# Optimization experiments

Hardware: AMD Instinct MI355X
Metric: run time of the kernel (lower is better)

The kernel has to match this reference:

```python
import jax, jax.numpy as jnp
import numpy as np

EMBEDDING_DIM = 128
NEG = -1000.0


def setup_inputs() -> dict:
    key = jax.random.key(0)
    ks = jax.random.split(key, 7)
    B, S_src, S_tgt, D = 2, 4096, 512, EMBEDDING_DIM
    return {
        "input_embeddings": jax.random.normal(ks[0], (B, S_src, D), dtype=jnp.float32),
        "token_attention_masks_source": jax.random.randint(ks[1], (B, S_src), 0, 2, dtype=jnp.int32),
        "token_attention_masks_target": jax.random.randint(ks[2], (B, S_tgt), 0, 2, dtype=jnp.int32),
        "encoder_output_embedding": jax.random.normal(ks[3], (B, S_tgt, D), dtype=jnp.float32),
        "w_query": jax.random.uniform(ks[4], (D, D), dtype=jnp.float32),
        "w_key": jax.random.uniform(ks[5], (D, D), dtype=jnp.float32),
        "w_value": jax.random.uniform(ks[6], (D, D), dtype=jnp.float32),
    }


def reference(input_embeddings, token_attention_masks_source,
              token_attention_masks_target, encoder_output_embedding,
              w_query, w_key, w_value):
    # Encoder self-attention branch (attention_type='encoder'), num_heads=1.
    D = w_query.shape[0]
    q = jnp.einsum('bsd,de->bse', input_embeddings, w_query)   # [B,S,D]
    k = jnp.einsum('bsd,de->bse', input_embeddings, w_key)     # [B,S,D]
    v = jnp.einsum('bsd,de->bse', input_embeddings, w_value)   # [B,S,D]
    scores = jnp.einsum('bsd,btd->bst', q, k) / jnp.sqrt(jnp.float32(D))
    # Original adds mask along the QUERY axis: mask[B,S] -> unsqueeze(-1).
    add_mask = jnp.where(token_attention_masks_source == 0, NEG, 0.0).astype(scores.dtype)
    scores = scores + add_mask[:, :, None]
    probs = jax.nn.softmax(scores, axis=2)                      # softmax over keys
    out = jnp.einsum('bst,btd->bsd', probs, v)                  # [B,S,D]
    return out
```

## Files before the change

### kernel.cpp

```cpp
#include <hip/hip_runtime.h>
#include <hip/hip_bf16.h>

#define S_SRC 4096
#define DIM 128
#define BATCH 2
#define NSP 8
#define NQB 32
#define NQG 512
#define NITER 16

typedef unsigned short u16;
typedef unsigned int u32;
typedef __bf16 bf16x8 __attribute__((ext_vector_type(8)));
typedef float f32x4 __attribute__((ext_vector_type(4)));
typedef u32 u32x4 __attribute__((ext_vector_type(4)));
typedef u16 u16x4 __attribute__((ext_vector_type(4)));

__device__ __forceinline__ __bf16 bf_hi(float x) { return (__bf16)x; }
__device__ __forceinline__ __bf16 bf_lo(float x, __bf16 h) { return (__bf16)(x - (float)h); }
__device__ __forceinline__ u16 bfu(__bf16 h) { return __builtin_bit_cast(u16, h); }
__device__ __forceinline__ u16 f2bu(float x) { return __builtin_bit_cast(u16, (__bf16)x); }
__device__ __forceinline__ float bu2f(u16 u) { return (float)__builtin_bit_cast(__bf16, u); }
__device__ __forceinline__ u32 pk2(float lo, float hi) {
  return (u32)f2bu(lo) | ((u32)f2bu(hi) << 16);
}
__device__ __forceinline__ void g2l16(const u16* src, u16* ldst) {
  __builtin_amdgcn_global_load_lds((const __attribute__((address_space(1))) void*)src,
                                   (__attribute__((address_space(3))) void*)ldst, 16, 0, 0);
}
#define MFMA __builtin_amdgcn_mfma_f32_16x16x32_bf16

__global__ __launch_bounds__(256) void k_wsplit(const float* __restrict__ wq,
                                                const float* __restrict__ wk,
                                                const float* __restrict__ wv,
                                                u16* __restrict__ wt) {
  int idx = blockIdx.x * 256 + threadIdx.x;
  int mat = idx >> 14;
  int r = idx & 16383;
  int d = r >> 7, e = r & 127;
  const float* w = (mat == 0) ? wq : ((mat == 1) ? wk : wv);
  float x = w[r];
  if (mat == 0) x *= 0.08838834764831845f;
  __bf16 h = bf_hi(x);
  __bf16 l = bf_lo(x, h);
  wt[((mat * 2 + 0) * 128 + e) * 128 + d] = bfu(h);
  wt[((mat * 2 + 1) * 128 + e) * 128 + d] = bfu(l);
}

__global__ __launch_bounds__(256) void k_proj(const float* __restrict__ X,
                                              const u16* __restrict__ wt,
                                              u16* __restrict__ Qh, u16* __restrict__ Ql,
                                              u16* __restrict__ Kh, u16* __restrict__ Kl,
                                              u16* __restrict__ VT) {
  const int mat = blockIdx.x >> 8;
  const int t = blockIdx.x & 255;
  const int b = t >> 7;
  const int tile = t & 127;
  const int tid = threadIdx.x;
  const int w = tid >> 6, lane = tid & 63, g = lane >> 4, l16 = lane & 15;

  bf16x8 a_h[2][4], a_l[2][4];
#pragma unroll
  for (int mf = 0; mf < 2; ++mf) {
    int row = tile * 32 + mf * 16 + l16;
    const float* xr = X + ((size_t)b * S_SRC + row) * DIM;
#pragma unroll
    for (int kf = 0; kf < 4; ++kf) {
      int d0 = kf * 32 + g * 8;
      f32x4 x0 = *(const f32x4*)(xr + d0);
      f32x4 x1 = *(const f32x4*)(xr + d0 + 4);
#pragma unroll
      for (int j = 0; j < 4; ++j) {
        __bf16 h0 = bf_hi(x0[j]);
        __bf16 h1 = bf_hi(x1[j]);
        a_h[mf][kf][j] = h0;
        a_l[mf][kf][j] = bf_lo(x0[j], h0);
        a_h[mf][kf][4 + j] = h1;
        a_l[mf][kf][4 + j] = bf_lo(x1[j], h1);
      }
    }
  }

  const u16* wth = wt + (mat * 2 + 0) * 16384;
  const u16* wtl = wt + (mat * 2 + 1) * 16384;
#pragma unroll
  for (int nf = 0; nf < 2; ++nf) {
    int col = w * 32 + nf * 16 + l16;
    f32x4 acc[2];
    acc[0] = (f32x4){0.f, 0.f, 0.f, 0.f};
    acc[1] = (f32x4){0.f, 0.f, 0.f, 0.f};
#pragma unroll
    for (int kf = 0; kf < 4; ++kf) {
      int d0 = kf * 32 + g * 8;
      bf16x8 bh = *(const bf16x8*)(const void*)(wth + col * 128 + d0);
      bf16x8 bl = *(const bf16x8*)(const void*)(wtl + col * 128 + d0);
#pragma unroll
      for (int mf = 0; mf < 2; ++mf) {
        acc[mf] = MFMA(a_h[mf][kf], bh, acc[mf], 0, 0, 0);
        acc[mf] = MFMA(a_h[mf][kf], bl, acc[mf], 0, 0, 0);
        acc[mf] = MFMA(a_l[mf][kf], bh, acc[mf], 0, 0, 0);
      }
    }
#pragma unroll
    for (int mf = 0; mf < 2; ++mf)
#pragma unroll
      for (int r = 0; r < 4; ++r) {
        int row = tile * 32 + mf * 16 + g * 4 + r;
        float v = acc[mf][r];
        if (mat == 2) {
          VT[((size_t)b * DIM + col) * S_SRC + row] = f2bu(v);
        } else {
          __bf16 h = bf_hi(v);
          __bf16 l = bf_lo(v, h);
          size_t o = ((size_t)b * S_SRC + row) * DIM + col;
          if (mat == 0) { Qh[o] = bfu(h); Ql[o] = bfu(l); }
          else          { Kh[o] = bfu(h); Kl[o] = bfu(l); }
        }
      }
  }
}

__device__ __forceinline__ void qk_tile(const u16* kb, int g, int l16,
                                        const bf16x8 qh0[4], const bf16x8 ql0[4],
                                        const bf16x8 qh1[4], const bf16x8 ql1[4],
                                        f32x4& s00, f32x4& s01, f32x4& s10, f32x4& s11) {
  s00 = s01 = s10 = s11 = (f32x4){0.f, 0.f, 0.f, 0.f};
  __builtin_amdgcn_s_setprio(1);
#pragma unroll
  for (int kf = 0; kf < 4; ++kf) {
    int cs = ((kf * 4 + g) ^ l16) << 3;
    bf16x8 kh0 = *(const bf16x8*)(const void*)(kb + l16 * 128 + cs);
    bf16x8 kl0 = *(const bf16x8*)(const void*)(kb + 4096 + l16 * 128 + cs);
    s00 = MFMA(kh0, qh0[kf], s00, 0, 0, 0);
    s00 = MFMA(kh0, ql0[kf], s00, 0, 0, 0);
    s00 = MFMA(kl0, qh0[kf], s00, 0, 0, 0);
    s10 = MFMA(kh0, qh1[kf], s10, 0, 0, 0);
    s10 = MFMA(kh0, ql1[kf], s10, 0, 0, 0);
    s10 = MFMA(kl0, qh1[kf], s10, 0, 0, 0);
    bf16x8 kh1 = *(const bf16x8*)(const void*)(kb + (16 + l16) * 128 + cs);
    bf16x8 kl1 = *(const bf16x8*)(const void*)(kb + 4096 + (16 + l16) * 128 + cs);
    s01 = MFMA(kh1, qh0[kf], s01, 0, 0, 0);
    s01 = MFMA(kh1, ql0[kf], s01, 0, 0, 0);
    s01 = MFMA(kl1, qh0[kf], s01, 0, 0, 0);
    s11 = MFMA(kh1, qh1[kf], s11, 0, 0, 0);
    s11 = MFMA(kh1, ql1[kf], s11, 0, 0, 0);
    s11 = MFMA(kl1, qh1[kf], s11, 0, 0, 0);
  }
  __builtin_amdgcn_s_setprio(0);
}

__device__ __forceinline__ void sm_pack(f32x4 sA, f32x4 sB, float& mr, float& lr,
                                        f32x4 acc[8], int g, bf16x8& pa) {
  float mx = fmaxf(fmaxf(fmaxf(sA[0], sA[1]), fmaxf(sA[2], sA[3])),
                   fmaxf(fmaxf(sB[0], sB[1]), fmaxf(sB[2], sB[3])));
  mx = fmaxf(mx, __shfl_xor(mx, 16, 64));
  mx = fmaxf(mx, __shfl_xor(mx, 32, 64));
  if (!__all(mx - mr <= 8.0f)) {
    float mn = fmaxf(mr, mx);
    float f = __expf(mr - mn);
    lr *= f;
    mr = mn;
    float fr0 = __shfl(f, g * 4 + 0, 64);
    float fr1 = __shfl(f, g * 4 + 1, 64);
    float fr2 = __shfl(f, g * 4 + 2, 64);
    float fr3 = __shfl(f, g * 4 + 3, 64);
#pragma unroll
    for (int nf = 0; nf < 8; ++nf) {
      acc[nf][0] *= fr0; acc[nf][1] *= fr1; acc[nf][2] *= fr2; acc[nf][3] *= fr3;
    }
  }
  float e0 = __expf(sA[0] - mr), e1 = __expf(sA[1] - mr);
  float e2 = __expf(sA[2] - mr), e3 = __expf(sA[3] - mr);
  float e4 = __expf(sB[0] - mr), e5 = __expf(sB[1] - mr);
  float e6 = __expf(sB[2] - mr), e7 = __expf(sB[3] - mr);
  float sm = ((e0 + e1) + (e2 + e3)) + ((e4 + e5) + (e6 + e7));
  sm += __shfl_xor(sm, 16, 64);
  sm += __shfl_xor(sm, 32, 64);
  lr += sm;
  u32 w0 = pk2(e0, e1), w1 = pk2(e2, e3), w2 = pk2(e4, e5), w3 = pk2(e6, e7);
  u32 x0 = __shfl_xor(w0, 16, 64), x1 = __shfl_xor(w1, 16, 64);
  u32 x2 = __shfl_xor(w2, 16, 64), x3 = __shfl_xor(w3, 16, 64);
  bool odd = (g & 1);
  u32x4 pw;
  pw.x = odd ? x2 : w0;
  pw.y = odd ? x3 : w1;
  pw.z = odd ? w2 : x0;
  pw.w = odd ? w3 : x1;
  pa = __builtin_bit_cast(bf16x8, pw);
}

__device__ __forceinline__ void pv_tile(const u16* vb, int mg, int l16,
                                        bf16x8 pa0, bf16x8 pa1,
                                        f32x4 acc0[8], f32x4 acc1[8]) {
  __builtin_amdgcn_s_setprio(1);
#pragma unroll
  for (int nf = 0; nf < 8; ++nf) {
    int d = nf * 16 + l16;
    bf16x8 vf = *(const bf16x8*)(const void*)(vb + d * 32 + ((mg ^ ((d >> 1) & 3)) << 3));
    acc0[nf] = MFMA(pa0, vf, acc0[nf], 0, 0, 0);
    acc1[nf] = MFMA(pa1, vf, acc1[nf], 0, 0, 0);
  }
  __builtin_amdgcn_s_setprio(0);
}

__global__ __launch_bounds__(512, 2) void k_attn(const u16* __restrict__ Qh, const u16* __restrict__ Ql,
                                                 const u16* __restrict__ Kh, const u16* __restrict__ Kl,
                                                 const u16* __restrict__ VT,
                                                 float* __restrict__ Pm, float* __restrict__ Pl,
                                                 u16* __restrict__ PO) {
  const int bid = blockIdx.x;
  const int sp = bid & 7;
  const int qb = bid >> 3;
  const int b = qb >> 4;
  const int tid = threadIdx.x;
  const int w = tid >> 6, lane = tid & 63, g = lane >> 4, l16 = lane & 15;

  __shared__ alignas(16) u16 kbuf[4][8192];
  __shared__ alignas(16) u16 vbuf[4][4096];

  const int gr0 = qb * 256 + w * 32;
  bf16x8 qh0[4], ql0[4], qh1[4], ql1[4];
  {
    const u16* p0h = Qh + ((size_t)gr0 + l16) * DIM;
    const u16* p0l = Ql + ((size_t)gr0 + l16) * DIM;
    const u16* p1h = Qh + ((size_t)gr0 + 16 + l16) * DIM;
    const u16* p1l = Ql + ((size_t)gr0 + 16 + l16) * DIM;
#pragma unroll
    for (int kf = 0; kf < 4; ++kf) {
      int d0 = kf * 32 + g * 8;
      qh0[kf] = *(const bf16x8*)(const void*)(p0h + d0);
      ql0[kf] = *(const bf16x8*)(const void*)(p0l + d0);
      qh1[kf] = *(const bf16x8*)(const void*)(p1h + d0);
      ql1[kf] = *(const bf16x8*)(const void*)(p1l + d0);
    }
  }

  f32x4 acc0[8], acc1[8];
#pragma unroll
  for (int nf = 0; nf < 8; ++nf) {
    acc0[nf] = (f32x4){0.f, 0.f, 0.f, 0.f};
    acc1[nf] = (f32x4){0.f, 0.f, 0.f, 0.f};
  }
  float m0 = -1e30f, m1 = -1e30f, l0 = 0.f, l1 = 0.f;

  const int key_base = sp * (S_SRC / NSP);
  const u16* KhB = Kh + (size_t)b * S_SRC * DIM;
  const u16* KlB = Kl + (size_t)b * S_SRC * DIM;
  const u16* VTB = VT + (size_t)b * DIM * S_SRC;

  const int kkey = tid >> 4, kcp = tid & 15;
  const int kcs = (kcp ^ (kkey & 15)) << 3;
  const int vd = tid >> 2, vcp = tid & 3;
  const int vcs = (vcp ^ ((vd >> 1) & 3)) << 3;
  const int wbase = w * 512;
  const int mg = ((g & 1) << 1) | (g >> 1);

#define STAGE(BUF, KEY0)                                                        \
  {                                                                             \
    g2l16(KhB + ((size_t)((KEY0) + kkey)) * DIM + kcs, &kbuf[BUF][wbase]);      \
    g2l16(KlB + ((size_t)((KEY0) + kkey)) * DIM + kcs, &kbuf[BUF][4096 + wbase]); \
    g2l16(VTB + (size_t)vd * S_SRC + (KEY0) + vcs,     &vbuf[BUF][wbase]);      \
  }
#define BODY(I)                                                                  \
  {                                                                              \
    f32x4 s00, s01, s10, s11;                                                    \
    qk_tile(kbuf[(I) & 3], g, l16, qh0, ql0, qh1, ql1, s00, s01, s10, s11);      \
    bf16x8 pa0, pa1;                                                             \
    sm_pack(s00, s01, m0, l0, acc0, g, pa0);                                     \
    sm_pack(s10, s11, m1, l1, acc1, g, pa1);                                     \
    pv_tile(vbuf[(I) & 3], mg, l16, pa0, pa1, acc0, acc1);                       \
  }

  STAGE(0, key_base)
  STAGE(1, key_base + 32)

  for (int i = 0; i < NITER - 2; ++i) {
    STAGE((i + 2) & 3, key_base + (i + 2) * 32)
    asm volatile("s_waitcnt vmcnt(6)" ::: "memory");
    __builtin_amdgcn_s_barrier();
    BODY(i)
  }
  asm volatile("s_waitcnt vmcnt(3)" ::: "memory");
  __builtin_amdgcn_s_barrier();
  BODY(NITER - 2)
  asm volatile("s_waitcnt vmcnt(0)" ::: "memory");
  __builtin_amdgcn_s_barrier();
  BODY(NITER - 1)

  const int pidx0 = sp * NQG + (gr0 >> 4);
  {
    u16* po = PO + (size_t)pidx0 * 16 * DIM;
#pragma unroll
    for (int nf = 0; nf < 8; ++nf)
#pragma unroll
      for (int r = 0; r < 4; ++r)
        po[(g * 4 + r) * DIM + nf * 16 + l16] = f2bu(acc0[nf][r]);
    u16* po1 = PO + (size_t)(pidx0 + 1) * 16 * DIM;
#pragma unroll
    for (int nf = 0; nf < 8; ++nf)
#pragma unroll
      for (int r = 0; r < 4; ++r)
        po1[(g * 4 + r) * DIM + nf * 16 + l16] = f2bu(acc1[nf][r]);
  }
  if (g == 0) { Pm[pidx0 * 16 + l16] = m0; Pl[pidx0 * 16 + l16] = l0; }
  if (g == 1) { Pm[(pidx0 + 1) * 16 + l16] = m1; Pl[(pidx0 + 1) * 16 + l16] = l1; }
#undef STAGE
#undef BODY
}

__global__ __launch_bounds__(64) void k_comb(const float* __restrict__ Pm,
                                             const float* __restrict__ Pl,
                                             const u16* __restrict__ PO,
                                             float* __restrict__ out) {
  const int qg = blockIdx.x;
  const int tid = threadIdx.x;

  __shared__ float sc[NSP][16];
  if (tid < 16) {
    float m = -1e30f;
#pragma unroll
    for (int s = 0; s < NSP; ++s) m = fmaxf(m, Pm[(s * NQG + qg) * 16 + tid]);
    float den = 0.f;
#pragma unroll
    for (int s = 0; s < NSP; ++s) {
      float e = __expf(Pm[(s * NQG + qg) * 16 + tid] - m);
      sc[s][tid] = e;
      den += Pl[(s * NQG + qg) * 16 + tid] * e;
    }
    float inv = 1.0f / den;
#pragma unroll
    for (int s = 0; s < NSP; ++s) sc[s][tid] *= inv;
  }
  __syncthreads();

  float* op = out + (size_t)qg * 16 * DIM;
  for (int i = tid; i < 16 * DIM / 4; i += 64) {
    int row = (i * 4) >> 7;
    f32x4 a = (f32x4){0.f, 0.f, 0.f, 0.f};
#pragma unroll
    for (int s = 0; s < NSP; ++s) {
      u16x4 p = *(const u16x4*)(const void*)(PO + (size_t)(s * NQG + qg) * 16 * DIM + i * 4);
      float wgt = sc[s][row];
      a[0] += bu2f(p.x) * wgt;
      a[1] += bu2f(p.y) * wgt;
      a[2] += bu2f(p.z) * wgt;
      a[3] += bu2f(p.w) * wgt;
    }
    *(f32x4*)(op + i * 4) = a;
  }
}

extern "C" void kernel_launch(void* const* d_in, const int* in_sizes, int n_in,
                              void* d_out, int out_size, void* d_ws, size_t ws_size,
                              hipStream_t stream) {
  const float* X  = (const float*)d_in[0];
  const float* wq = (const float*)d_in[4];
  const float* wk = (const float*)d_in[5];
  const float* wv = (const float*)d_in[6];
  float* out = (float*)d_out;

  u16* WT = (u16*)d_ws;
  u16* Qh = WT + 3 * 2 * 128 * 128;
  u16* Ql = Qh + (size_t)BATCH * S_SRC * DIM;
  u16* Kh = Ql + (size_t)BATCH * S_SRC * DIM;
  u16* Kl = Kh + (size_t)BATCH * S_SRC * DIM;
  u16* VT = Kl + (size_t)BATCH * S_SRC * DIM;
  float* Pm = (float*)(VT + (size_t)BATCH * S_SRC * DIM);
  float* Pl = Pm + (size_t)NSP * NQG * 16;
  u16* PO = (u16*)(Pl + (size_t)NSP * NQG * 16);

  hipLaunchKernelGGL(k_wsplit, dim3(192), dim3(256), 0, stream, wq, wk, wv, WT);
  hipLaunchKernelGGL(k_proj, dim3(3 * 256), dim3(256), 0, stream,
                     X, WT, Qh, Ql, Kh, Kl, VT);
  hipLaunchKernelGGL(k_attn, dim3(NQB * NSP), dim3(512), 0, stream,
                     Qh, Ql, Kh, Kl, VT, Pm, Pl, PO);
  hipLaunchKernelGGL(k_comb, dim3(NQG), dim3(64), 0, stream, Pm, Pl, PO, out);
}
```

Baseline: 74.60 us.

## Process 64-key windows with triple-buffered LDS instead of 32-key quad buffers

Each iteration of the attention loop now handles 64 keys instead of 32, halving the number of barriers and online-softmax max/sum reductions. The LDS pipeline moves from 4 buffers of 32 keys to 3 buffers of 64 keys, with the prefetch issued after the barrier. This raises register pressure (more score accumulators live) and LDS use, which may affect occupancy at 2 blocks per CU.

```diff
diff --git a/kernel.cpp b/kernel.cpp
--- a/kernel.cpp
+++ b/kernel.cpp
@@ -7,7 +7,7 @@
 #define NSP 8
 #define NQB 32
 #define NQG 512
-#define NITER 16
+#define NWIN 8
 
 typedef unsigned short u16;
 typedef unsigned int u32;
@@ -120,89 +120,6 @@
   }
 }
 
-__device__ __forceinline__ void qk_tile(const u16* kb, int g, int l16,
-                                        const bf16x8 qh0[4], const bf16x8 ql0[4],
-                                        const bf16x8 qh1[4], const bf16x8 ql1[4],
-                                        f32x4& s00, f32x4& s01, f32x4& s10, f32x4& s11) {
-  s00 = s01 = s10 = s11 = (f32x4){0.f, 0.f, 0.f, 0.f};
-  __builtin_amdgcn_s_setprio(1);
-#pragma unroll
-  for (int kf = 0; kf < 4; ++kf) {
-    int cs = ((kf * 4 + g) ^ l16) << 3;
-    bf16x8 kh0 = *(const bf16x8*)(const void*)(kb + l16 * 128 + cs);
-    bf16x8 kl0 = *(const bf16x8*)(const void*)(kb + 4096 + l16 * 128 + cs);
-    s00 = MFMA(kh0, qh0[kf], s00, 0, 0, 0);
-    s00 = MFMA(kh0, ql0[kf], s00, 0, 0, 0);
-    s00 = MFMA(kl0, qh0[kf], s00, 0, 0, 0);
-    s10 = MFMA(kh0, qh1[kf], s10, 0, 0, 0);
-    s10 = MFMA(kh0, ql1[kf], s10, 0, 0, 0);
-    s10 = MFMA(kl0, qh1[kf], s10, 0, 0, 0);
-    bf16x8 kh1 = *(const bf16x8*)(const void*)(kb + (16 + l16) * 128 + cs);
-    bf16x8 kl1 = *(const bf16x8*)(const void*)(kb + 4096 + (16 + l16) * 128 + cs);
-    s01 = MFMA(kh1, qh0[kf], s01, 0, 0, 0);
-    s01 = MFMA(kh1, ql0[kf], s01, 0, 0, 0);
-    s01 = MFMA(kl1, qh0[kf], s01, 0, 0, 0);
-    s11 = MFMA(kh1, qh1[kf], s11, 0, 0, 0);
-    s11 = MFMA(kh1, ql1[kf], s11, 0, 0, 0);
-    s11 = MFMA(kl1, qh1[kf], s11, 0, 0, 0);
-  }
-  __builtin_amdgcn_s_setprio(0);
-}
-
-__device__ __forceinline__ void sm_pack(f32x4 sA, f32x4 sB, float& mr, float& lr,
-                                        f32x4 acc[8], int g, bf16x8& pa) {
-  float mx = fmaxf(fmaxf(fmaxf(sA[0], sA[1]), fmaxf(sA[2], sA[3])),
-                   fmaxf(fmaxf(sB[0], sB[1]), fmaxf(sB[2], sB[3])));
-  mx = fmaxf(mx, __shfl_xor(mx, 16, 64));
-  mx = fmaxf(mx, __shfl_xor(mx, 32, 64));
-  if (!__all(mx - mr <= 8.0f)) {
-    float mn = fmaxf(mr, mx);
-    float f = __expf(mr - mn);
-    lr *= f;
-    mr = mn;
-    float fr0 = __shfl(f, g * 4 + 0, 64);
-    float fr1 = __shfl(f, g * 4 + 1, 64);
-    float fr2 = __shfl(f, g * 4 + 2, 64);
-    float fr3 = __shfl(f, g * 4 + 3, 64);
-#pragma unroll
-    for (int nf = 0; nf < 8; ++nf) {
-      acc[nf][0] *= fr0; acc[nf][1] *= fr1; acc[nf][2] *= fr2; acc[nf][3] *= fr3;
-    }
-  }
-  float e0 = __expf(sA[0] - mr), e1 = __expf(sA[1] - mr);
-  float e2 = __expf(sA[2] - mr), e3 = __expf(sA[3] - mr);
-  float e4 = __expf(sB[0] - mr), e5 = __expf(sB[1] - mr);
-  float e6 = __expf(sB[2] - mr), e7 = __expf(sB[3] - mr);
-  float sm = ((e0 + e1) + (e2 + e3)) + ((e4 + e5) + (e6 + e7));
-  sm += __shfl_xor(sm, 16, 64);
-  sm += __shfl_xor(sm, 32, 64);
-  lr += sm;
-  u32 w0 = pk2(e0, e1), w1 = pk2(e2, e3), w2 = pk2(e4, e5), w3 = pk2(e6, e7);
-  u32 x0 = __shfl_xor(w0, 16, 64), x1 = __shfl_xor(w1, 16, 64);
-  u32 x2 = __shfl_xor(w2, 16, 64), x3 = __shfl_xor(w3, 16, 64);
-  bool odd = (g & 1);
-  u32x4 pw;
-  pw.x = odd ? x2 : w0;
-  pw.y = odd ? x3 : w1;
-  pw.z = odd ? w2 : x0;
-  pw.w = odd ? w3 : x1;
-  pa = __builtin_bit_cast(bf16x8, pw);
-}
-
-__device__ __forceinline__ void pv_tile(const u16* vb, int mg, int l16,
-                                        bf16x8 pa0, bf16x8 pa1,
-                                        f32x4 acc0[8], f32x4 acc1[8]) {
-  __builtin_amdgcn_s_setprio(1);
-#pragma unroll
-  for (int nf = 0; nf < 8; ++nf) {
-    int d = nf * 16 + l16;
-    bf16x8 vf = *(const bf16x8*)(const void*)(vb + d * 32 + ((mg ^ ((d >> 1) & 3)) << 3));
-    acc0[nf] = MFMA(pa0, vf, acc0[nf], 0, 0, 0);
-    acc1[nf] = MFMA(pa1, vf, acc1[nf], 0, 0, 0);
-  }
-  __builtin_amdgcn_s_setprio(0);
-}
-
 __global__ __launch_bounds__(512, 2) void k_attn(const u16* __restrict__ Qh, const u16* __restrict__ Ql,
                                                  const u16* __restrict__ Kh, const u16* __restrict__ Kl,
                                                  const u16* __restrict__ VT,
@@ -215,8 +132,8 @@
   const int tid = threadIdx.x;
   const int w = tid >> 6, lane = tid & 63, g = lane >> 4, l16 = lane & 15;
 
-  __shared__ alignas(16) u16 kbuf[4][8192];
-  __shared__ alignas(16) u16 vbuf[4][4096];
+  __shared__ alignas(16) u16 kbuf[3][16384];
+  __shared__ alignas(16) u16 vbuf[3][8192];
 
   const int gr0 = qb * 256 + w * 32;
   bf16x8 qh0[4], ql0[4], qh1[4], ql1[4];
@@ -248,44 +165,145 @@
   const u16* KlB = Kl + (size_t)b * S_SRC * DIM;
   const u16* VTB = VT + (size_t)b * DIM * S_SRC;
 
-  const int kkey = tid >> 4, kcp = tid & 15;
-  const int kcs = (kcp ^ (kkey & 15)) << 3;
-  const int vd = tid >> 2, vcp = tid & 3;
-  const int vcs = (vcp ^ ((vd >> 1) & 3)) << 3;
-  const int wbase = w * 512;
+  const int kkey0 = tid >> 4;
+  const int kks = ((tid & 15) ^ (kkey0 & 15)) << 3;
+  const int vd0 = tid >> 3;
+  const int vks = ((tid & 7) ^ ((vd0 >> 1) & 7)) << 3;
+  const int wb = w * 512;
   const int mg = ((g & 1) << 1) | (g >> 1);
 
-#define STAGE(BUF, KEY0)                                                        \
-  {                                                                             \
-    g2l16(KhB + ((size_t)((KEY0) + kkey)) * DIM + kcs, &kbuf[BUF][wbase]);      \
-    g2l16(KlB + ((size_t)((KEY0) + kkey)) * DIM + kcs, &kbuf[BUF][4096 + wbase]); \
-    g2l16(VTB + (size_t)vd * S_SRC + (KEY0) + vcs,     &vbuf[BUF][wbase]);      \
-  }
-#define BODY(I)                                                                  \
-  {                                                                              \
-    f32x4 s00, s01, s10, s11;                                                    \
-    qk_tile(kbuf[(I) & 3], g, l16, qh0, ql0, qh1, ql1, s00, s01, s10, s11);      \
-    bf16x8 pa0, pa1;                                                             \
-    sm_pack(s00, s01, m0, l0, acc0, g, pa0);                                     \
-    sm_pack(s10, s11, m1, l1, acc1, g, pa1);                                     \
-    pv_tile(vbuf[(I) & 3], mg, l16, pa0, pa1, acc0, acc1);                       \
+#define STAGE(BUF, KEY0)                                                             \
+  {                                                                                  \
+    g2l16(KhB + ((size_t)((KEY0) + kkey0)) * DIM + kks,      &kbuf[BUF][wb]);        \
+    g2l16(KhB + ((size_t)((KEY0) + 32 + kkey0)) * DIM + kks, &kbuf[BUF][4096 + wb]); \
+    g2l16(KlB + ((size_t)((KEY0) + kkey0)) * DIM + kks,      &kbuf[BUF][8192 + wb]); \
+    g2l16(KlB + ((size_t)((KEY0) + 32 + kkey0)) * DIM + kks, &kbuf[BUF][12288 + wb]);\
+    g2l16(VTB + (size_t)vd0 * S_SRC + (KEY0) + vks,          &vbuf[BUF][wb]);        \
+    g2l16(VTB + (size_t)(64 + vd0) * S_SRC + (KEY0) + vks,   &vbuf[BUF][4096 + wb]); \
+  }
+
+#define SMPACK(S, MR, LR, ACC, PA, PB)                                               \
+  {                                                                                  \
+    float mxa = fmaxf(fmaxf(fmaxf(S[0][0], S[0][1]), fmaxf(S[0][2], S[0][3])),       \
+                      fmaxf(fmaxf(S[1][0], S[1][1]), fmaxf(S[1][2], S[1][3])));      \
+    float mxb = fmaxf(fmaxf(fmaxf(S[2][0], S[2][1]), fmaxf(S[2][2], S[2][3])),       \
+                      fmaxf(fmaxf(S[3][0], S[3][1]), fmaxf(S[3][2], S[3][3])));      \
+    float mx = fmaxf(mxa, mxb);                                                      \
+    mx = fmaxf(mx, __shfl_xor(mx, 16, 64));                                          \
+    mx = fmaxf(mx, __shfl_xor(mx, 32, 64));                                          \
+    if (!__all(mx - MR <= 8.0f)) {                                                   \
+      float mn = fmaxf(MR, mx);                                                      \
+      float f = __expf(MR - mn);                                                     \
+      LR *= f; MR = mn;                                                              \
+      float fr0 = __shfl(f, g * 4 + 0, 64);                                          \
+      float fr1 = __shfl(f, g * 4 + 1, 64);                                          \
+      float fr2 = __shfl(f, g * 4 + 2, 64);                                          \
+      float fr3 = __shfl(f, g * 4 + 3, 64);                                          \
+      _Pragma("unroll")                                                              \
+      for (int nf = 0; nf < 8; ++nf) {                                               \
+        ACC[nf][0] *= fr0; ACC[nf][1] *= fr1;                                        \
+        ACC[nf][2] *= fr2; ACC[nf][3] *= fr3;                                        \
+      }                                                                              \
+    }                                                                                \
+    float e0 = __expf(S[0][0] - MR), e1 = __expf(S[0][1] - MR);                      \
+    float e2 = __expf(S[0][2] - MR), e3 = __expf(S[0][3] - MR);                      \
+    float e4 = __expf(S[1][0] - MR), e5 = __expf(S[1][1] - MR);                      \
+    float e6 = __expf(S[1][2] - MR), e7 = __expf(S[1][3] - MR);                      \
+    float f0 = __expf(S[2][0] - MR), f1 = __expf(S[2][1] - MR);                      \
+    float f2 = __expf(S[2][2] - MR), f3 = __expf(S[2][3] - MR);                      \
+    float f4 = __expf(S[3][0] - MR), f5 = __expf(S[3][1] - MR);                      \
+    float f6 = __expf(S[3][2] - MR), f7 = __expf(S[3][3] - MR);                      \
+    float sm = (((e0 + e1) + (e2 + e3)) + ((e4 + e5) + (e6 + e7)))                   \
+             + (((f0 + f1) + (f2 + f3)) + ((f4 + f5) + (f6 + f7)));                  \
+    sm += __shfl_xor(sm, 16, 64);                                                    \
+    sm += __shfl_xor(sm, 32, 64);                                                    \
+    LR += sm;                                                                        \
+    bool odd = (g & 1);                                                              \
+    {                                                                                \
+      u32 w0 = pk2(e0, e1), w1 = pk2(e2, e3), w2 = pk2(e4, e5), w3 = pk2(e6, e7);    \
+      u32 x0 = __shfl_xor(w0, 16, 64), x1 = __shfl_xor(w1, 16, 64);                  \
+      u32 x2 = __shfl_xor(w2, 16, 64), x3 = __shfl_xor(w3, 16, 64);                  \
+      u32x4 pw;                                                                      \
+      pw.x = odd ? x2 : w0; pw.y = odd ? x3 : w1;                                    \
+      pw.z = odd ? w2 : x0; pw.w = odd ? w3 : x1;                                    \
+      PA = __builtin_bit_cast(bf16x8, pw);                                           \
+    }                                                                                \
+    {                                                                                \
+      u32 w0 = pk2(f0, f1), w1 = pk2(f2, f3), w2 = pk2(f4, f5), w3 = pk2(f6, f7);    \
+      u32 x0 = __shfl_xor(w0, 16, 64), x1 = __shfl_xor(w1, 16, 64);                  \
+      u32 x2 = __shfl_xor(w2, 16, 64), x3 = __shfl_xor(w3, 16, 64);                  \
+      u32x4 pw;                                                                      \
+      pw.x = odd ? x2 : w0; pw.y = odd ? x3 : w1;                                    \
+      pw.z = odd ? w2 : x0; pw.w = odd ? w3 : x1;                                    \
+      PB = __builtin_bit_cast(bf16x8, pw);                                           \
+    }                                                                                \
   }
 
   STAGE(0, key_base)
-  STAGE(1, key_base + 32)
-
-  for (int i = 0; i < NITER - 2; ++i) {
-    STAGE((i + 2) & 3, key_base + (i + 2) * 32)
-    asm volatile("s_waitcnt vmcnt(6)" ::: "memory");
+  STAGE(1, key_base + 64)
+
+  int cur = 0;
+  for (int i = 0; i < NWIN; ++i) {
+    if (i < NWIN - 1) {
+      asm volatile("s_waitcnt vmcnt(6)" ::: "memory");
+    } else {
+      asm volatile("s_waitcnt vmcnt(0)" ::: "memory");
+    }
     __builtin_amdgcn_s_barrier();
-    BODY(i)
-  }
-  asm volatile("s_waitcnt vmcnt(3)" ::: "memory");
-  __builtin_amdgcn_s_barrier();
-  BODY(NITER - 2)
-  asm volatile("s_waitcnt vmcnt(0)" ::: "memory");
-  __builtin_amdgcn_s_barrier();
-  BODY(NITER - 1)
+    if (i + 2 < NWIN) {
+      int nx = cur + 2; nx = (nx >= 3) ? nx - 3 : nx;
+      STAGE(nx, key_base + (i + 2) * 64)
+    }
+
+    const u16* kb = kbuf[cur];
+    const u16* vb = vbuf[cur];
+
+    f32x4 sg0[4], sg1[4];
+#pragma unroll
+    for (int st = 0; st < 4; ++st) {
+      sg0[st] = (f32x4){0.f, 0.f, 0.f, 0.f};
+      sg1[st] = (f32x4){0.f, 0.f, 0.f, 0.f};
+    }
+    __builtin_amdgcn_s_setprio(1);
+#pragma unroll
+    for (int kf = 0; kf < 4; ++kf) {
+      int cs = ((kf * 4 + g) ^ l16) << 3;
+#pragma unroll
+      for (int st = 0; st < 4; ++st) {
+        const u16* kp = kb + (st * 16 + l16) * 128 + cs;
+        bf16x8 kh = *(const bf16x8*)(const void*)kp;
+        bf16x8 kl = *(const bf16x8*)(const void*)(kp + 8192);
+        sg0[st] = MFMA(kh, qh0[kf], sg0[st], 0, 0, 0);
+        sg0[st] = MFMA(kh, ql0[kf], sg0[st], 0, 0, 0);
+        sg0[st] = MFMA(kl, qh0[kf], sg0[st], 0, 0, 0);
+        sg1[st] = MFMA(kh, qh1[kf], sg1[st], 0, 0, 0);
+        sg1[st] = MFMA(kh, ql1[kf], sg1[st], 0, 0, 0);
+        sg1[st] = MFMA(kl, qh1[kf], sg1[st], 0, 0, 0);
+      }
+    }
+    __builtin_amdgcn_s_setprio(0);
+
+    bf16x8 pa0A, pa0B, pa1A, pa1B;
+    SMPACK(sg0, m0, l0, acc0, pa0A, pa0B)
+    SMPACK(sg1, m1, l1, acc1, pa1A, pa1B)
+
+    __builtin_amdgcn_s_setprio(1);
+#pragma unroll
+    for (int nf = 0; nf < 8; ++nf) {
+      int d = nf * 16 + l16;
+      int sw = (d >> 1) & 7;
+      const u16* vr = vb + d * 64;
+      bf16x8 vf0 = *(const bf16x8*)(const void*)(vr + ((mg ^ sw) << 3));
+      bf16x8 vf1 = *(const bf16x8*)(const void*)(vr + (((4 + mg) ^ sw) << 3));
+      acc0[nf] = MFMA(pa0A, vf0, acc0[nf], 0, 0, 0);
+      acc0[nf] = MFMA(pa0B, vf1, acc0[nf], 0, 0, 0);
+      acc1[nf] = MFMA(pa1A, vf0, acc1[nf], 0, 0, 0);
+      acc1[nf] = MFMA(pa1B, vf1, acc1[nf], 0, 0, 0);
+    }
+    __builtin_amdgcn_s_setprio(0);
+
+    cur = (cur + 1 >= 3) ? cur - 2 : cur + 1;
+  }
 
   const int pidx0 = sp * NQG + (gr0 >> 4);
   {
@@ -305,7 +323,7 @@
   if (g == 0) { Pm[pidx0 * 16 + l16] = m0; Pl[pidx0 * 16 + l16] = l0; }
   if (g == 1) { Pm[(pidx0 + 1) * 16 + l16] = m1; Pl[(pidx0 + 1) * 16 + l16] = l1; }
 #undef STAGE
-#undef BODY
+#undef SMPACK
 }
 
 __global__ __launch_bounds__(64) void k_comb(const float* __restrict__ Pm,
```

Result: faster. 72.54 us (-2.8%).
